# Kernel optimization log

Hardware: AMD Instinct MI355X
Metric: run time of the kernel (lower is better)

The kernel has to match this reference:

```python
import jax, jax.numpy as jnp
import numpy as np

CHUNK_SIZE = 256


def setup_inputs() -> dict:
    key = jax.random.key(0)
    kq, kk, kv = jax.random.split(key, 3)
    b, h, L, d, dv = 2, 16, 4096, 16, 64
    return {
        "q": jax.random.normal(kq, (b, h, L, d), dtype=jnp.float32),
        "k": jax.random.normal(kk, (b, h, L, d), dtype=jnp.float32),
        "v": jax.random.normal(kv, (b, h, L, dv), dtype=jnp.float32),
    }


def reference(q, k, v):
    b, h, L, d = q.shape
    dv = v.shape[-1]
    cs = CHUNK_SIZE
    n = L // cs

    q = q * d ** (-0.5)

    # ---- normalizer z over full sequence ----
    k_cumsum = jnp.cumsum(k, axis=-2)                               # [b,h,L,d]
    kk_cumsum = jnp.cumsum(k[..., :, None] * k[..., None, :], axis=-3)  # [b,h,L,d,d]
    z = (q * k_cumsum).sum(-1)
    z = z + 0.5 * jnp.einsum('bhld,bhle,bhlde->bhl', q, q, kk_cumsum)
    z = z + (jnp.arange(L, dtype=z.dtype) + 1.0)[None, None, :]

    # ---- zeroth-order term ----
    o_const = jnp.cumsum(v, axis=-2)                                # [b,h,L,dv]

    # ---- chunked view ----
    qc = q.reshape(b, h, n, cs, d)
    kc = k.reshape(b, h, n, cs, d)
    vc = v.reshape(b, h, n, cs, dv)

    # intra-chunk quadratic attention: S + 0.5*S^2, causal-masked
    s = jnp.einsum('bhnqd,bhnkd->bhnqk', qc, kc)                    # [b,h,n,cs,cs]
    s = s + 0.5 * s ** 2
    causal_mask = jnp.tril(jnp.ones((cs, cs), dtype=bool))
    s = jnp.where(causal_mask, s, jnp.zeros((), dtype=s.dtype))
    o = jnp.einsum('bhnqk,bhnkf->bhnqf', s, vc)                     # [b,h,n,cs,dv]

    # inter-chunk quadratic state: cumulative K x K x V from previous chunks
    kv_quad = jnp.einsum('bhncd,bhnce,bhncf->bhndef', kc, kc, vc)   # [b,h,n,d,d,dv]
    kv_quad = jnp.cumsum(kv_quad, axis=2)
    kv_quad = jnp.concatenate(
        [jnp.zeros_like(kv_quad[:, :, :1]), kv_quad[:, :, :-1]], axis=2)
    o = o + 0.5 * jnp.einsum('bhndef,bhncd,bhnce->bhncf', kv_quad, qc, qc)

    # inter-chunk linear state: cumulative K x V from previous chunks
    kv_lin = jnp.einsum('bhncd,bhnce->bhnde', kc, vc)               # [b,h,n,d,dv]
    kv_lin = jnp.cumsum(kv_lin, axis=2)
    kv_lin = jnp.concatenate(
        [jnp.zeros_like(kv_lin[:, :, :1]), kv_lin[:, :, :-1]], axis=2)
    o = o + jnp.einsum('bhnde,bhncd->bhnce', kv_lin, qc)

    o = o.reshape(b, h, L, dv) + o_const
    return o / (z[..., None] + 1e-6)
```

## Files before the change

### kernel.cpp

```cpp
#include <hip/hip_runtime.h>
#include <hip/hip_cooperative_groups.h>
#include <cstddef>

#define BH    32
#define LSEQ  4096
#define D     16
#define DV    64
#define CS    256
#define NC    16
#define NF    160
#define NZ    65
#define KSTEPS 5
#define PER   (NZ * NF)

typedef short short8 __attribute__((ext_vector_type(8)));
typedef float f32x4 __attribute__((ext_vector_type(4)));

#define OFF_KBF 0u
#define OFF_VT  (4u*1024u*1024u)
#define OFF_ST  (OFF_VT + (unsigned)(BH*NZ*LSEQ*2))

__device__ __forceinline__ unsigned f2bf(float x) {
  unsigned u = __float_as_uint(x);
  return (u + 0x7FFFu + ((u >> 16) & 1u)) >> 16;
}
__device__ __forceinline__ float bf2f(unsigned short u) {
  return __uint_as_float(((unsigned)u) << 16);
}
__device__ __forceinline__ short8 zero8() {
  short8 z = {0,0,0,0,0,0,0,0};
  return z;
}

__device__ __forceinline__ unsigned feat_tbl(int f) {
  if (f == 0)  return 16u | (16u << 8);
  if (f <= 16) return (unsigned)(f - 1) | (16u << 8);
  if (f < 137) {
    int p = f - 17, off = 0;
    for (int d = 0; d < 15; ++d) {
      int cnt = 15 - d;
      if (p < off + cnt) return (unsigned)d | ((unsigned)(d + 1 + p - off) << 8);
      off += cnt;
    }
  }
  if (f < 153) {
    int d = f - 137;
    return (unsigned)d | ((unsigned)d << 8) | (1u << 16);
  }
  return 17u | (17u << 8);
}

struct SmemA {
  float kx[CS][18];
  __align__(16) unsigned short vt[NZ][264];
};
struct SmemC {
  float qx[CS][18];
  __align__(16) unsigned short st[NZ][168];
  __align__(16) unsigned short ptile[8][1280];
  float zline[CS];
};
union SmemU { SmemA a; SmemC c; };

__global__ __launch_bounds__(512, 4) void unified(const float* __restrict__ q,
                                                  const float* __restrict__ k,
                                                  const float* __restrict__ v,
                                                  unsigned* __restrict__ kbf_u32,
                                                  unsigned* __restrict__ vt_u32,
                                                  unsigned short* __restrict__ st,
                                                  float* __restrict__ out) {
  __shared__ SmemU sm;
  __shared__ unsigned tbl[NF];
  int blk = blockIdx.x, bh = blk >> 4, c = blk & 15;
  int t = threadIdx.x, w = t >> 6, lane = t & 63, quad = lane >> 4, n16 = lane & 15;
  const size_t base = (size_t)bh * LSEQ + (size_t)c * CS;

  {
    const float2* kc2 = (const float2*)(k + base * D);
    unsigned* kbd = kbf_u32 + base * D / 2;
    for (int i = t; i < 2048; i += 512) {
      float2 v2 = kc2[i];
      kbd[i] = f2bf(v2.x) | (f2bf(v2.y) << 16);
      int j = i >> 3, dd = (i & 7) * 2;
      sm.a.kx[j][dd] = v2.x; sm.a.kx[j][dd + 1] = v2.y;
    }
    for (int i = t; i < CS; i += 512) { sm.a.kx[i][16] = 1.f; sm.a.kx[i][17] = 0.f; }
    const float* vb = v + base * DV;
    for (int i = t; i < CS * DV; i += 512) {
      int j = i >> 6, f = i & 63;
      sm.a.vt[f][j] = (unsigned short)f2bf(vb[i]);
    }
    for (int i = t; i < CS; i += 512) sm.a.vt[64][i] = (unsigned short)0x3F80;
    if (t < NF) tbl[t] = feat_tbl(t);
  }
  __syncthreads();
  {
    unsigned* vtg = vt_u32 + (size_t)bh * NZ * (LSEQ / 2) + c * (CS / 2);
    for (int i = t; i < NZ * (CS / 2); i += 512) {
      int f = i >> 7, jp = (i & 127) * 2;
      vtg[(size_t)f * (LSEQ / 2) + (i & 127)] =
          (unsigned)sm.a.vt[f][jp] | ((unsigned)sm.a.vt[f][jp + 1] << 16);
    }
  }
  if (w < 5) {
    f32x4 acc[2][5];
#pragma unroll
    for (int mm = 0; mm < 2; ++mm)
#pragma unroll
      for (int nt = 0; nt < 5; ++nt) acc[mm][nt] = (f32x4){0.f, 0.f, 0.f, 0.f};
    for (int jt = 0; jt < 8; ++jt) {
      short8 afr[2];
#pragma unroll
      for (int mm = 0; mm < 2; ++mm) {
        int feat = (w * 2 + mm) * 16 + n16;
        unsigned tv = tbl[feat];
        int d = tv & 255, e = (tv >> 8) & 255;
        short8 a;
#pragma unroll
        for (int i = 0; i < 8; ++i) {
          int jj = jt * 32 + quad * 8 + i;
          a[i] = (short)f2bf(sm.a.kx[jj][d] * sm.a.kx[jj][e]);
        }
        afr[mm] = a;
      }
#pragma unroll
      for (int nt = 0; nt < 5; ++nt) {
        int ncol = nt * 16 + n16;
        short8 b = zero8();
        if (ncol < NZ) b = *(const short8*)(&sm.a.vt[ncol][jt * 32 + quad * 8]);
        acc[0][nt] = __builtin_amdgcn_mfma_f32_16x16x32_bf16(afr[0], b, acc[0][nt], 0, 0, 0);
        acc[1][nt] = __builtin_amdgcn_mfma_f32_16x16x32_bf16(afr[1], b, acc[1][nt], 0, 0, 0);
      }
    }
    unsigned short* stc = st + (size_t)(bh * NC + c) * PER;
#pragma unroll
    for (int mm = 0; mm < 2; ++mm)
#pragma unroll
      for (int nt = 0; nt < 5; ++nt) {
        int col = nt * 16 + n16;
        if (col < NZ) {
          unsigned lo = f2bf(acc[mm][nt][0]) | (f2bf(acc[mm][nt][1]) << 16);
          unsigned hi = f2bf(acc[mm][nt][2]) | (f2bf(acc[mm][nt][3]) << 16);
          int feat0 = (w * 2 + mm) * 16 + quad * 4;
          *(uint2*)(stc + (size_t)col * NF + feat0) = make_uint2(lo, hi);
        }
      }
  }

  cooperative_groups::this_grid().sync();

  {
    const float* qc = q + base * D;
    for (int i = t; i < CS * D; i += 512) {
      int row = i >> 4, dd = i & 15;
      sm.c.qx[row][dd] = qc[i] * 0.25f;
    }
    for (int i = t; i < CS; i += 512) { sm.c.qx[i][16] = 1.f; sm.c.qx[i][17] = 0.f; }
    if (c > 0) {
      const unsigned short* stg = st + (size_t)bh * NC * PER;
      for (int i = t; i < PER; i += 512) {
        float s = 0.f;
        for (int cc = 0; cc < c; ++cc) s += bf2f(stg[(size_t)cc * PER + i]);
        int col = i / NF, ft = i - col * NF;
        sm.c.st[col][ft] = (unsigned short)f2bf(s);
      }
    }
  }
  __syncthreads();

  f32x4 acc[2][5];
#pragma unroll
  for (int mm = 0; mm < 2; ++mm)
#pragma unroll
    for (int nt = 0; nt < 5; ++nt) acc[mm][nt] = (f32x4){0.f, 0.f, 0.f, 0.f};

  if (c > 0) {
    for (int ks = 0; ks < KSTEPS; ++ks) {
      short8 afr[2];
#pragma unroll
      for (int mm = 0; mm < 2; ++mm) {
        const float* qrow = sm.c.qx[(w * 2 + mm) * 16 + n16];
        short8 a;
#pragma unroll
        for (int i = 0; i < 8; ++i) {
          int f = ks * 32 + quad * 8 + i;
          unsigned tv = tbl[f];
          float val = qrow[tv & 255] * qrow[(tv >> 8) & 255];
          if (tv & 0x10000u) val *= 0.5f;
          a[i] = (short)f2bf(val);
        }
        afr[mm] = a;
      }
#pragma unroll
      for (int nt = 0; nt < 5; ++nt) {
        int ncol = nt * 16 + n16;
        short8 b = zero8();
        if (ncol < NZ) b = *(const short8*)(&sm.c.st[ncol][ks * 32 + quad * 8]);
        acc[0][nt] = __builtin_amdgcn_mfma_f32_16x16x32_bf16(afr[0], b, acc[0][nt], 0, 0, 0);
        acc[1][nt] = __builtin_amdgcn_mfma_f32_16x16x32_bf16(afr[1], b, acc[1][nt], 0, 0, 0);
      }
    }
  }

  short8 qfr[2];
#pragma unroll
  for (int mm = 0; mm < 2; ++mm) {
    int m = (w * 2 + mm) * 16 + n16;
    short8 a = zero8();
    if (quad < 2) {
#pragma unroll
      for (int i = 0; i < 8; ++i) a[i] = (short)f2bf(sm.c.qx[m][quad * 8 + i]);
    }
    qfr[mm] = a;
  }
  const unsigned short* kbc = (const unsigned short*)kbf_u32 + base * D;
  const unsigned short* vtb = (const unsigned short*)vt_u32 + (size_t)bh * NZ * LSEQ + (size_t)c * CS;
  unsigned short* pw = &sm.c.ptile[w][0];
  short8 ones;
#pragma unroll
  for (int i = 0; i < 8; ++i) ones[i] = (short)0x3F80;

  for (int jt = 0; jt <= w; ++jt) {
    short8 kb[2];
#pragma unroll
    for (int ntk = 0; ntk < 2; ++ntk) {
      short8 b = zero8();
      if (quad < 2)
        b = *(const short8*)(kbc + (size_t)(jt * 32 + ntk * 16 + n16) * D + quad * 8);
      kb[ntk] = b;
    }
    f32x4 zf = (f32x4){0.f, 0.f, 0.f, 0.f};
    f32x4 s[2][2];
#pragma unroll
    for (int mm = 0; mm < 2; ++mm)
#pragma unroll
      for (int ntk = 0; ntk < 2; ++ntk)
        s[mm][ntk] = __builtin_amdgcn_mfma_f32_16x16x32_bf16(qfr[mm], kb[ntk], zf, 0, 0, 0);
    bool diag = (jt == w);
#pragma unroll
    for (int mm = 0; mm < 2; ++mm)
#pragma unroll
      for (int ntk = 0; ntk < 2; ++ntk)
#pragma unroll
        for (int r = 0; r < 4; ++r) {
          float sv = s[mm][ntk][r];
          float phi = fmaf(0.5f * sv, sv, sv) + 1.0f;
          if (diag) {
            int qrow = mm * 16 + quad * 4 + r;
            int kcol = ntk * 16 + n16;
            if (kcol > qrow) phi = 0.f;
          }
          pw[(mm * 16 + quad * 4 + r) * 40 + ntk * 16 + n16] = (unsigned short)f2bf(phi);
        }
    short8 pa[2];
#pragma unroll
    for (int mm = 0; mm < 2; ++mm)
      pa[mm] = *(const short8*)(pw + (mm * 16 + n16) * 40 + quad * 8);
#pragma unroll
    for (int nt = 0; nt < 5; ++nt) {
      int ncol = nt * 16 + n16;
      short8 b;
      if (ncol < 64)       b = *(const short8*)(vtb + (size_t)ncol * LSEQ + jt * 32 + quad * 8);
      else if (ncol == 64) b = ones;
      else                 b = zero8();
      acc[0][nt] = __builtin_amdgcn_mfma_f32_16x16x32_bf16(pa[0], b, acc[0][nt], 0, 0, 0);
      acc[1][nt] = __builtin_amdgcn_mfma_f32_16x16x32_bf16(pa[1], b, acc[1][nt], 0, 0, 0);
    }
  }

  if (n16 == 0) {
#pragma unroll
    for (int mm = 0; mm < 2; ++mm)
#pragma unroll
      for (int r = 0; r < 4; ++r)
        sm.c.zline[(w * 2 + mm) * 16 + quad * 4 + r] = acc[mm][4][r];
  }
  float* oc = out + base * DV;
#pragma unroll
  for (int mm = 0; mm < 2; ++mm)
#pragma unroll
    for (int r = 0; r < 4; ++r) {
      int qrow = (w * 2 + mm) * 16 + quad * 4 + r;
      float inv = 1.0f / (sm.c.zline[qrow] + 1e-6f);
#pragma unroll
      for (int nt = 0; nt < 4; ++nt)
        oc[(size_t)qrow * DV + nt * 16 + n16] = acc[mm][nt][r] * inv;
    }
}

__global__ __launch_bounds__(320) void pass_a(const float* __restrict__ k,
                                              const float* __restrict__ v,
                                              unsigned* __restrict__ kbf_u32,
                                              unsigned* __restrict__ vt_u32,
                                              unsigned short* __restrict__ st) {
  __shared__ float kx[CS][18];
  __shared__ __align__(16) unsigned short vt_lds[NZ][264];
  __shared__ unsigned tbl[NF];
  int blk = blockIdx.x, bh = blk >> 4, c = blk & 15;
  int t = threadIdx.x, w = t >> 6, lane = t & 63, quad = lane >> 4, n16 = lane & 15;
  {
    const float2* kc2 = (const float2*)(k + ((size_t)bh * LSEQ + c * CS) * D);
    unsigned* kbd = kbf_u32 + ((size_t)bh * LSEQ + c * CS) * D / 2;
    for (int i = t; i < 2048; i += 320) {
      float2 v2 = kc2[i];
      kbd[i] = f2bf(v2.x) | (f2bf(v2.y) << 16);
      int j = i >> 3, dd = (i & 7) * 2;
      kx[j][dd] = v2.x; kx[j][dd + 1] = v2.y;
    }
    for (int i = t; i < CS; i += 320) { kx[i][16] = 1.f; kx[i][17] = 0.f; }
  }
  {
    const float* vb = v + ((size_t)bh * LSEQ + c * CS) * DV;
    for (int i = t; i < CS * DV; i += 320) {
      int j = i >> 6, f = i & 63;
      vt_lds[f][j] = (unsigned short)f2bf(vb[i]);
    }
    for (int i = t; i < CS; i += 320) vt_lds[64][i] = (unsigned short)0x3F80;
  }
  if (t < NF) tbl[t] = feat_tbl(t);
  __syncthreads();
  {
    unsigned* vtg = vt_u32 + (size_t)bh * NZ * (LSEQ / 2) + c * (CS / 2);
    for (int i = t; i < NZ * (CS / 2); i += 320) {
      int f = i >> 7, jp = (i & 127) * 2;
      vtg[(size_t)f * (LSEQ / 2) + (i & 127)] =
          (unsigned)vt_lds[f][jp] | ((unsigned)vt_lds[f][jp + 1] << 16);
    }
  }
  f32x4 acc[2][5];
#pragma unroll
  for (int mm = 0; mm < 2; ++mm)
#pragma unroll
    for (int nt = 0; nt < 5; ++nt) acc[mm][nt] = (f32x4){0.f, 0.f, 0.f, 0.f};
  for (int jt = 0; jt < 8; ++jt) {
    short8 afr[2];
#pragma unroll
    for (int mm = 0; mm < 2; ++mm) {
      int feat = (w * 2 + mm) * 16 + n16;
      unsigned tv = tbl[feat];
      int d = tv & 255, e = (tv >> 8) & 255;
      short8 a;
#pragma unroll
      for (int i = 0; i < 8; ++i) {
        int jj = jt * 32 + quad * 8 + i;
        a[i] = (short)f2bf(kx[jj][d] * kx[jj][e]);
      }
      afr[mm] = a;
    }
#pragma unroll
    for (int nt = 0; nt < 5; ++nt) {
      int ncol = nt * 16 + n16;
      short8 b = zero8();
      if (ncol < NZ) b = *(const short8*)(&vt_lds[ncol][jt * 32 + quad * 8]);
      acc[0][nt] = __builtin_amdgcn_mfma_f32_16x16x32_bf16(afr[0], b, acc[0][nt], 0, 0, 0);
      acc[1][nt] = __builtin_amdgcn_mfma_f32_16x16x32_bf16(afr[1], b, acc[1][nt], 0, 0, 0);
    }
  }
  unsigned short* stc = st + (size_t)(bh * NC + c) * PER;
#pragma unroll
  for (int mm = 0; mm < 2; ++mm)
#pragma unroll
    for (int nt = 0; nt < 5; ++nt) {
      int col = nt * 16 + n16;
      if (col < NZ) {
        unsigned lo = f2bf(acc[mm][nt][0]) | (f2bf(acc[mm][nt][1]) << 16);
        unsigned hi = f2bf(acc[mm][nt][2]) | (f2bf(acc[mm][nt][3]) << 16);
        int feat0 = (w * 2 + mm) * 16 + quad * 4;
        *(uint2*)(stc + (size_t)col * NF + feat0) = make_uint2(lo, hi);
      }
    }
}

__global__ __launch_bounds__(256) void pass_b(unsigned short* __restrict__ st) {
  const int TOT = BH * PER;
  int idx = blockIdx.x * 256 + threadIdx.x;
  if (idx >= TOT) return;
  int bh = idx / PER, r = idx - bh * PER;
  unsigned short* p = st + (size_t)bh * NC * PER + r;
  float run = 0.f;
#pragma unroll
  for (int c = 0; c < NC; ++c) {
    unsigned short uv = p[(size_t)c * PER];
    float val = bf2f(uv);
    p[(size_t)c * PER] = (unsigned short)f2bf(run);
    run += val;
  }
}

__global__ __launch_bounds__(512) void pass_c(const float* __restrict__ q,
                                              const unsigned short* __restrict__ kbf,
                                              const unsigned short* __restrict__ vt,
                                              const unsigned short* __restrict__ st,
                                              float* __restrict__ out) {
  __shared__ float qx[CS][18];
  __shared__ unsigned tbl[NF];
  __shared__ __align__(16) unsigned short ptile[8][32 * 40];
  __shared__ float zline[CS];
  int blk = blockIdx.x, bh = blk >> 4, c = blk & 15;
  const size_t base = (size_t)bh * LSEQ + (size_t)c * CS;
  const float* qc = q + base * D;
  int t = threadIdx.x, w = t >> 6, lane = t & 63, quad = lane >> 4, n16 = lane & 15;
  for (int i = t; i < CS * D; i += 512) {
    int row = i >> 4, dd = i & 15;
    qx[row][dd] = qc[i] * 0.25f;
  }
  for (int i = t; i < CS; i += 512) { qx[i][16] = 1.f; qx[i][17] = 0.f; }
  if (t < NF) tbl[t] = feat_tbl(t);
  __syncthreads();
  f32x4 acc[2][5];
#pragma unroll
  for (int mm = 0; mm < 2; ++mm)
#pragma unroll
    for (int nt = 0; nt < 5; ++nt) acc[mm][nt] = (f32x4){0.f, 0.f, 0.f, 0.f};
  if (c > 0) {
    const unsigned short* stc = st + (size_t)(bh * NC + c) * PER;
    for (int ks = 0; ks < KSTEPS; ++ks) {
      short8 afr[2];
#pragma unroll
      for (int mm = 0; mm < 2; ++mm) {
        const float* qrow = qx[(w * 2 + mm) * 16 + n16];
        short8 a;
#pragma unroll
        for (int i = 0; i < 8; ++i) {
          int f = ks * 32 + quad * 8 + i;
          unsigned tv = tbl[f];
          float val = qrow[tv & 255] * qrow[(tv >> 8) & 255];
          if (tv & 0x10000u) val *= 0.5f;
          a[i] = (short)f2bf(val);
        }
        afr[mm] = a;
      }
#pragma unroll
      for (int nt = 0; nt < 5; ++nt) {
        int ncol = nt * 16 + n16;
        short8 b = zero8();
        if (ncol < NZ) b = *(const short8*)(stc + (size_t)ncol * NF + ks * 32 + quad * 8);
        acc[0][nt] = __builtin_amdgcn_mfma_f32_16x16x32_bf16(afr[0], b, acc[0][nt], 0, 0, 0);
        acc[1][nt] = __builtin_amdgcn_mfma_f32_16x16x32_bf16(afr[1], b, acc[1][nt], 0, 0, 0);
      }
    }
  }
  short8 qfr[2];
#pragma unroll
  for (int mm = 0; mm < 2; ++mm) {
    int m = (w * 2 + mm) * 16 + n16;
    short8 a = zero8();
    if (quad < 2) {
#pragma unroll
      for (int i = 0; i < 8; ++i) a[i] = (short)f2bf(qx[m][quad * 8 + i]);
    }
    qfr[mm] = a;
  }
  const unsigned short* kbc = kbf + base * D;
  const unsigned short* vtb = vt + (size_t)bh * NZ * LSEQ + (size_t)c * CS;
  unsigned short* pw = &ptile[w][0];
  short8 ones;
#pragma unroll
  for (int i = 0; i < 8; ++i) ones[i] = (short)0x3F80;
  for (int jt = 0; jt <= w; ++jt) {
    short8 kb[2];
#pragma unroll
    for (int ntk = 0; ntk < 2; ++ntk) {
      short8 b = zero8();
      if (quad < 2)
        b = *(const short8*)(kbc + (size_t)(jt * 32 + ntk * 16 + n16) * D + quad * 8);
      kb[ntk] = b;
    }
    f32x4 zf = (f32x4){0.f, 0.f, 0.f, 0.f};
    f32x4 s[2][2];
#pragma unroll
    for (int mm = 0; mm < 2; ++mm)
#pragma unroll
      for (int ntk = 0; ntk < 2; ++ntk)
        s[mm][ntk] = __builtin_amdgcn_mfma_f32_16x16x32_bf16(qfr[mm], kb[ntk], zf, 0, 0, 0);
    bool diag = (jt == w);
#pragma unroll
    for (int mm = 0; mm < 2; ++mm)
#pragma unroll
      for (int ntk = 0; ntk < 2; ++ntk)
#pragma unroll
        for (int r = 0; r < 4; ++r) {
          float sv = s[mm][ntk][r];
          float phi = fmaf(0.5f * sv, sv, sv) + 1.0f;
          if (diag) {
            int qrow = mm * 16 + quad * 4 + r;
            int kcol = ntk * 16 + n16;
            if (kcol > qrow) phi = 0.f;
          }
          pw[(mm * 16 + quad * 4 + r) * 40 + ntk * 16 + n16] = (unsigned short)f2bf(phi);
        }
    short8 pa[2];
#pragma unroll
    for (int mm = 0; mm < 2; ++mm)
      pa[mm] = *(const short8*)(pw + (mm * 16 + n16) * 40 + quad * 8);
#pragma unroll
    for (int nt = 0; nt < 5; ++nt) {
      int ncol = nt * 16 + n16;
      short8 b;
      if (ncol < 64)       b = *(const short8*)(vtb + (size_t)ncol * LSEQ + jt * 32 + quad * 8);
      else if (ncol == 64) b = ones;
      else                 b = zero8();
      acc[0][nt] = __builtin_amdgcn_mfma_f32_16x16x32_bf16(pa[0], b, acc[0][nt], 0, 0, 0);
      acc[1][nt] = __builtin_amdgcn_mfma_f32_16x16x32_bf16(pa[1], b, acc[1][nt], 0, 0, 0);
    }
  }
  if (n16 == 0) {
#pragma unroll
    for (int mm = 0; mm < 2; ++mm)
#pragma unroll
      for (int r = 0; r < 4; ++r)
        zline[(w * 2 + mm) * 16 + quad * 4 + r] = acc[mm][4][r];
  }
  float* oc = out + base * DV;
#pragma unroll
  for (int mm = 0; mm < 2; ++mm)
#pragma unroll
    for (int r = 0; r < 4; ++r) {
      int qrow = (w * 2 + mm) * 16 + quad * 4 + r;
      float inv = 1.0f / (zline[qrow] + 1e-6f);
#pragma unroll
      for (int nt = 0; nt < 4; ++nt)
        oc[(size_t)qrow * DV + nt * 16 + n16] = acc[mm][nt][r] * inv;
    }
}

extern "C" void kernel_launch(void* const* d_in, const int* in_sizes, int n_in,
                              void* d_out, int out_size, void* d_ws, size_t ws_size,
                              hipStream_t stream) {
  (void)in_sizes; (void)n_in; (void)out_size; (void)ws_size;
  const float* q = (const float*)d_in[0];
  const float* k = (const float*)d_in[1];
  const float* v = (const float*)d_in[2];
  float* out = (float*)d_out;
  char* wsb = (char*)d_ws;
  unsigned*       kbf32 = (unsigned*)(wsb + OFF_KBF);
  unsigned short* kbf   = (unsigned short*)(wsb + OFF_KBF);
  unsigned*       vt32  = (unsigned*)(wsb + OFF_VT);
  unsigned short* vtp   = (unsigned short*)(wsb + OFF_VT);
  unsigned short* stp   = (unsigned short*)(wsb + OFF_ST);

  int nb = 0;
  hipError_t oe = hipOccupancyMaxActiveBlocksPerMultiprocessor(
      &nb, reinterpret_cast<const void*>(unified), 512, 0);
  if (oe == hipSuccess && nb >= 2) {
    void* args[] = {(void*)&q, (void*)&k, (void*)&v,
                    (void*)&kbf32, (void*)&vt32, (void*)&stp, (void*)&out};
    hipLaunchCooperativeKernel(reinterpret_cast<const void*>(unified),
                               dim3(BH * NC), dim3(512), args, 0, stream);
  } else {
    pass_a<<<BH * NC, 320, 0, stream>>>(k, v, kbf32, vt32, stp);
    pass_b<<<1300, 256, 0, stream>>>(stp);
    pass_c<<<BH * NC, 512, 0, stream>>>(q, kbf, vtp, stp, out);
  }
}
```

Measured before the change: 134.4 us.

## Keep V tile in LDS across grid sync, vectorize prefix-state reduction

```diff
diff --git a/kernel.cpp b/kernel.cpp
--- a/kernel.cpp
+++ b/kernel.cpp
@@ -50,27 +50,26 @@
   return 17u | (17u << 8);
 }
 
-struct SmemA {
-  float kx[CS][18];
+struct Smem {
+  float kxqx[CS][18];
   __align__(16) unsigned short vt[NZ][264];
+  union {
+    __align__(16) unsigned short stt[NZ][168];
+    struct {
+      __align__(16) unsigned short ptile[8][1280];
+      float zline[CS];
+    } u;
+  } b;
+  unsigned tbl[NF];
 };
-struct SmemC {
-  float qx[CS][18];
-  __align__(16) unsigned short st[NZ][168];
-  __align__(16) unsigned short ptile[8][1280];
-  float zline[CS];
-};
-union SmemU { SmemA a; SmemC c; };
 
 __global__ __launch_bounds__(512, 4) void unified(const float* __restrict__ q,
                                                   const float* __restrict__ k,
                                                   const float* __restrict__ v,
                                                   unsigned* __restrict__ kbf_u32,
-                                                  unsigned* __restrict__ vt_u32,
                                                   unsigned short* __restrict__ st,
                                                   float* __restrict__ out) {
-  __shared__ SmemU sm;
-  __shared__ unsigned tbl[NF];
+  __shared__ Smem sm;
   int blk = blockIdx.x, bh = blk >> 4, c = blk & 15;
   int t = threadIdx.x, w = t >> 6, lane = t & 63, quad = lane >> 4, n16 = lane & 15;
   const size_t base = (size_t)bh * LSEQ + (size_t)c * CS;
@@ -82,27 +81,20 @@
       float2 v2 = kc2[i];
       kbd[i] = f2bf(v2.x) | (f2bf(v2.y) << 16);
       int j = i >> 3, dd = (i & 7) * 2;
-      sm.a.kx[j][dd] = v2.x; sm.a.kx[j][dd + 1] = v2.y;
-    }
-    for (int i = t; i < CS; i += 512) { sm.a.kx[i][16] = 1.f; sm.a.kx[i][17] = 0.f; }
+      sm.kxqx[j][dd] = v2.x; sm.kxqx[j][dd + 1] = v2.y;
+    }
+    for (int i = t; i < CS; i += 512) { sm.kxqx[i][16] = 1.f; sm.kxqx[i][17] = 0.f; }
     const float* vb = v + base * DV;
     for (int i = t; i < CS * DV; i += 512) {
       int j = i >> 6, f = i & 63;
-      sm.a.vt[f][j] = (unsigned short)f2bf(vb[i]);
-    }
-    for (int i = t; i < CS; i += 512) sm.a.vt[64][i] = (unsigned short)0x3F80;
-    if (t < NF) tbl[t] = feat_tbl(t);
+      sm.vt[f][j] = (unsigned short)f2bf(vb[i]);
+    }
+    for (int i = t; i < CS; i += 512) sm.vt[64][i] = (unsigned short)0x3F80;
+    if (t < NF) sm.tbl[t] = feat_tbl(t);
   }
   __syncthreads();
-  {
-    unsigned* vtg = vt_u32 + (size_t)bh * NZ * (LSEQ / 2) + c * (CS / 2);
-    for (int i = t; i < NZ * (CS / 2); i += 512) {
-      int f = i >> 7, jp = (i & 127) * 2;
-      vtg[(size_t)f * (LSEQ / 2) + (i & 127)] =
-          (unsigned)sm.a.vt[f][jp] | ((unsigned)sm.a.vt[f][jp + 1] << 16);
-    }
-  }
-  if (w < 5) {
+
+  if (c < 15 && w < 5) {
     f32x4 acc[2][5];
 #pragma unroll
     for (int mm = 0; mm < 2; ++mm)
@@ -113,13 +105,13 @@
 #pragma unroll
       for (int mm = 0; mm < 2; ++mm) {
         int feat = (w * 2 + mm) * 16 + n16;
-        unsigned tv = tbl[feat];
+        unsigned tv = sm.tbl[feat];
         int d = tv & 255, e = (tv >> 8) & 255;
         short8 a;
 #pragma unroll
         for (int i = 0; i < 8; ++i) {
           int jj = jt * 32 + quad * 8 + i;
-          a[i] = (short)f2bf(sm.a.kx[jj][d] * sm.a.kx[jj][e]);
+          a[i] = (short)f2bf(sm.kxqx[jj][d] * sm.kxqx[jj][e]);
         }
         afr[mm] = a;
       }
@@ -127,7 +119,7 @@
       for (int nt = 0; nt < 5; ++nt) {
         int ncol = nt * 16 + n16;
         short8 b = zero8();
-        if (ncol < NZ) b = *(const short8*)(&sm.a.vt[ncol][jt * 32 + quad * 8]);
+        if (ncol < NZ) b = *(const short8*)(&sm.vt[ncol][jt * 32 + quad * 8]);
         acc[0][nt] = __builtin_amdgcn_mfma_f32_16x16x32_bf16(afr[0], b, acc[0][nt], 0, 0, 0);
         acc[1][nt] = __builtin_amdgcn_mfma_f32_16x16x32_bf16(afr[1], b, acc[1][nt], 0, 0, 0);
       }
@@ -146,23 +138,52 @@
         }
       }
   }
-
-  cooperative_groups::this_grid().sync();
+  __syncthreads();
 
   {
     const float* qc = q + base * D;
     for (int i = t; i < CS * D; i += 512) {
       int row = i >> 4, dd = i & 15;
-      sm.c.qx[row][dd] = qc[i] * 0.25f;
-    }
-    for (int i = t; i < CS; i += 512) { sm.c.qx[i][16] = 1.f; sm.c.qx[i][17] = 0.f; }
-    if (c > 0) {
-      const unsigned short* stg = st + (size_t)bh * NC * PER;
-      for (int i = t; i < PER; i += 512) {
-        float s = 0.f;
-        for (int cc = 0; cc < c; ++cc) s += bf2f(stg[(size_t)cc * PER + i]);
-        int col = i / NF, ft = i - col * NF;
-        sm.c.st[col][ft] = (unsigned short)f2bf(s);
+      sm.kxqx[row][dd] = qc[i] * 0.25f;
+    }
+  }
+
+  cooperative_groups::this_grid().sync();
+
+  if (c > 0) {
+    const unsigned short* stg = st + (size_t)bh * NC * PER;
+    float s0[8], s1[8], s2[8];
+#pragma unroll
+    for (int e = 0; e < 8; ++e) { s0[e] = 0.f; s1[e] = 0.f; s2[e] = 0.f; }
+    const int i0 = t * 8, i1 = i0 + 4096, i2 = i0 + 8192;
+    const bool h2 = (i2 < PER);
+    for (int cc = 0; cc < c; ++cc) {
+      const unsigned short* pcc = stg + (size_t)cc * PER;
+      short8 a0 = *(const short8*)(pcc + i0);
+      short8 a1 = *(const short8*)(pcc + i1);
+      short8 a2 = h2 ? *(const short8*)(pcc + i2) : zero8();
+#pragma unroll
+      for (int e = 0; e < 8; ++e) {
+        s0[e] += bf2f((unsigned short)a0[e]);
+        s1[e] += bf2f((unsigned short)a1[e]);
+        s2[e] += bf2f((unsigned short)a2[e]);
+      }
+    }
+    {
+      int col = i0 / NF, ft = i0 - col * NF;
+      short8 p;
+#pragma unroll
+      for (int e = 0; e < 8; ++e) p[e] = (short)f2bf(s0[e]);
+      *(short8*)(&sm.b.stt[col][ft]) = p;
+      col = i1 / NF; ft = i1 - col * NF;
+#pragma unroll
+      for (int e = 0; e < 8; ++e) p[e] = (short)f2bf(s1[e]);
+      *(short8*)(&sm.b.stt[col][ft]) = p;
+      if (h2) {
+        col = i2 / NF; ft = i2 - col * NF;
+#pragma unroll
+        for (int e = 0; e < 8; ++e) p[e] = (short)f2bf(s2[e]);
+        *(short8*)(&sm.b.stt[col][ft]) = p;
       }
     }
   }
@@ -179,12 +200,12 @@
       short8 afr[2];
 #pragma unroll
       for (int mm = 0; mm < 2; ++mm) {
-        const float* qrow = sm.c.qx[(w * 2 + mm) * 16 + n16];
+        const float* qrow = sm.kxqx[(w * 2 + mm) * 16 + n16];
         short8 a;
 #pragma unroll
         for (int i = 0; i < 8; ++i) {
           int f = ks * 32 + quad * 8 + i;
-          unsigned tv = tbl[f];
+          unsigned tv = sm.tbl[f];
           float val = qrow[tv & 255] * qrow[(tv >> 8) & 255];
           if (tv & 0x10000u) val *= 0.5f;
           a[i] = (short)f2bf(val);
@@ -195,12 +216,13 @@
       for (int nt = 0; nt < 5; ++nt) {
         int ncol = nt * 16 + n16;
         short8 b = zero8();
-        if (ncol < NZ) b = *(const short8*)(&sm.c.st[ncol][ks * 32 + quad * 8]);
+        if (ncol < NZ) b = *(const short8*)(&sm.b.stt[ncol][ks * 32 + quad * 8]);
         acc[0][nt] = __builtin_amdgcn_mfma_f32_16x16x32_bf16(afr[0], b, acc[0][nt], 0, 0, 0);
         acc[1][nt] = __builtin_amdgcn_mfma_f32_16x16x32_bf16(afr[1], b, acc[1][nt], 0, 0, 0);
       }
     }
   }
+  __syncthreads();
 
   short8 qfr[2];
 #pragma unroll
@@ -209,13 +231,12 @@
     short8 a = zero8();
     if (quad < 2) {
 #pragma unroll
-      for (int i = 0; i < 8; ++i) a[i] = (short)f2bf(sm.c.qx[m][quad * 8 + i]);
+      for (int i = 0; i < 8; ++i) a[i] = (short)f2bf(sm.kxqx[m][quad * 8 + i]);
     }
     qfr[mm] = a;
   }
   const unsigned short* kbc = (const unsigned short*)kbf_u32 + base * D;
-  const unsigned short* vtb = (const unsigned short*)vt_u32 + (size_t)bh * NZ * LSEQ + (size_t)c * CS;
-  unsigned short* pw = &sm.c.ptile[w][0];
+  unsigned short* pw = &sm.b.u.ptile[w][0];
   short8 ones;
 #pragma unroll
   for (int i = 0; i < 8; ++i) ones[i] = (short)0x3F80;
@@ -260,7 +281,7 @@
     for (int nt = 0; nt < 5; ++nt) {
       int ncol = nt * 16 + n16;
       short8 b;
-      if (ncol < 64)       b = *(const short8*)(vtb + (size_t)ncol * LSEQ + jt * 32 + quad * 8);
+      if (ncol < 64)       b = *(const short8*)(&sm.vt[ncol][jt * 32 + quad * 8]);
       else if (ncol == 64) b = ones;
       else                 b = zero8();
       acc[0][nt] = __builtin_amdgcn_mfma_f32_16x16x32_bf16(pa[0], b, acc[0][nt], 0, 0, 0);
@@ -273,7 +294,7 @@
     for (int mm = 0; mm < 2; ++mm)
 #pragma unroll
       for (int r = 0; r < 4; ++r)
-        sm.c.zline[(w * 2 + mm) * 16 + quad * 4 + r] = acc[mm][4][r];
+        sm.b.u.zline[(w * 2 + mm) * 16 + quad * 4 + r] = acc[mm][4][r];
   }
   float* oc = out + base * DV;
 #pragma unroll
@@ -281,7 +302,7 @@
 #pragma unroll
     for (int r = 0; r < 4; ++r) {
       int qrow = (w * 2 + mm) * 16 + quad * 4 + r;
-      float inv = 1.0f / (sm.c.zline[qrow] + 1e-6f);
+      float inv = 1.0f / (sm.b.u.zline[qrow] + 1e-6f);
 #pragma unroll
       for (int nt = 0; nt < 4; ++nt)
         oc[(size_t)qrow * DV + nt * 16 + n16] = acc[mm][nt][r] * inv;
@@ -544,7 +565,7 @@
       &nb, reinterpret_cast<const void*>(unified), 512, 0);
   if (oe == hipSuccess && nb >= 2) {
     void* args[] = {(void*)&q, (void*)&k, (void*)&v,
-                    (void*)&kbf32, (void*)&vt32, (void*)&stp, (void*)&out};
+                    (void*)&kbf32, (void*)&stp, (void*)&out};
     hipLaunchCooperativeKernel(reinterpret_cast<const void*>(unified),
                                dim3(BH * NC), dim3(512), args, 0, stream);
   } else {
```

Measured after the change: 130.1 us. -3.3%, faster.
